# Optimization experiments

Hardware: AMD Instinct MI355X
Metric: run time of the kernel (lower is better)

The kernel has to match this reference:

```python
import jax, jax.numpy as jnp
import numpy as np

EPS = 1e-8
LN_EPS = 1e-5
CAPACITY_BETA = 1.5
IDEAL_CLASSES = 5.0

B, F, E, H, C, G = 8192, 1024, 30, 256, 100, 4096


def setup_inputs() -> dict:
    key = jax.random.key(0)
    ks = jax.random.split(key, 8)
    x = jax.random.normal(ks[0], (B, F), dtype=jnp.float32)
    prototypes = jax.random.normal(ks[1], (E, F), dtype=jnp.float32)
    g_new = jax.random.normal(ks[2], (G,), dtype=jnp.float32)
    g_mem = jax.random.normal(ks[3], (E, G), dtype=jnp.float32)
    class_counts = jax.random.randint(ks[4], (E,), 0, 12, dtype=jnp.int32)
    W1 = jax.random.normal(ks[5], (E, F, H), dtype=jnp.float32) * (1.0 / np.sqrt(F))
    b1 = jnp.zeros((E, H), dtype=jnp.float32)
    gamma = jnp.ones((E, H), dtype=jnp.float32)
    beta = jnp.zeros((E, H), dtype=jnp.float32)
    W2 = jax.random.normal(ks[6], (E, H, C), dtype=jnp.float32) * (1.0 / np.sqrt(H))
    b2 = jnp.zeros((E, C), dtype=jnp.float32)
    return {"x": x, "prototypes": prototypes, "g_new": g_new, "g_mem": g_mem,
            "class_counts": class_counts, "W1": W1, "b1": b1, "gamma": gamma,
            "beta": beta, "W2": W2, "b2": b2}


def _route_scores(x, prototypes, g_new, g_mem, class_counts):
    # Cosine similarity of each sample to each expert prototype: [B, E]
    xn = x / (jnp.linalg.norm(x, axis=-1, keepdims=True) + EPS)
    pn = prototypes / (jnp.linalg.norm(prototypes, axis=-1, keepdims=True) + EPS)
    sim = xn @ pn.T
    # Gradient alignment score per expert (cosine of new grad vs EMA memory), mapped to [0, 1]
    gn = g_new / (jnp.linalg.norm(g_new) + EPS)
    gm = g_mem / (jnp.linalg.norm(g_mem, axis=-1, keepdims=True) + EPS)
    align = 0.5 * (1.0 + gm @ gn)  # [E]
    # Capacity penalty: exponential decay once an expert exceeds its ideal class load
    overload = jnp.maximum(class_counts.astype(jnp.float32) / IDEAL_CLASSES - 1.0, 0.0)
    capacity = jnp.exp(-CAPACITY_BETA * overload)  # [E]
    return sim * (align * capacity)[None, :]  # [B, E]


def reference(x, prototypes, g_new, g_mem, class_counts, W1, b1, gamma, beta, W2, b2):
    scores = _route_scores(x, prototypes, g_new, g_mem, class_counts)  # [B, E]
    assign = jnp.argmax(scores, axis=-1)  # [B] expert id per sample
    # Expert MLP: Linear -> LayerNorm -> GELU -> Linear, evaluated for all experts
    h = jnp.einsum('bf,efh->ebh', x, W1) + b1[:, None, :]  # [E, B, H]
    mu = h.mean(axis=-1, keepdims=True)
    var = ((h - mu) ** 2).mean(axis=-1, keepdims=True)
    ln = (h - mu) * jax.lax.rsqrt(var + LN_EPS) * gamma[:, None, :] + beta[:, None, :]
    a = jax.nn.gelu(ln, approximate=False)  # torch nn.GELU default is exact erf
    logits_all = jnp.einsum('ebh,ehc->ebc', a, W2) + b2[:, None, :]  # [E, B, C]
    # Dispatch: each sample keeps only its assigned expert's logits
    logits = logits_all[assign, jnp.arange(x.shape[0])]  # [B, C]
    return logits
```

## Files before the change

### kernel.cpp

```cpp
#include <hip/hip_runtime.h>
#include <hip/hip_bf16.h>
#include <math.h>
#include <float.h>

namespace {
constexpr int Bn = 8192;
constexpr int Fn = 1024;
constexpr int En = 30;
constexpr int Hn = 256;
constexpr int Cn = 100;
constexpr int Gn = 4096;
constexpr int TILECAP64 = 158;
constexpr int TILECAP32 = 285;
constexpr float EPSF  = 1e-8f;
constexpr float LNEPS = 1e-5f;

typedef _Float16 f16x8 __attribute__((ext_vector_type(8)));
typedef float    f32x4 __attribute__((ext_vector_type(4)));

__device__ __forceinline__ int bswz(int k) { return (k & 7) ^ ((k >> 3) << 2); }
}

#define GLDS16(g, s) __builtin_amdgcn_global_load_lds(                         \
    (const __attribute__((address_space(1))) void*)(uintptr_t)(g),             \
    (__attribute__((address_space(3))) void*)(uintptr_t)(s), 16, 0, 0)

__global__ __launch_bounds__(256) void k_route_w(
    const float* __restrict__ protos,
    const float* __restrict__ g_new,
    const float* __restrict__ g_mem,
    const int* __restrict__ ccounts,
    float* __restrict__ w,
    int* __restrict__ cnt) {
  const int e = blockIdx.x, t = threadIdx.x;
  if (e == 0 && t < 32) cnt[t] = 0;
  float d = 0.f, gm2 = 0.f, gn2 = 0.f, p2 = 0.f;
  for (int g = t; g < Gn; g += 256) {
    float a = g_new[g];
    float m = g_mem[(size_t)e * Gn + g];
    d += a * m; gm2 += m * m; gn2 += a * a;
  }
  for (int f = t; f < Fn; f += 256) {
    float v = protos[(size_t)e * Fn + f];
    p2 += v * v;
  }
#pragma unroll
  for (int m = 1; m < 64; m <<= 1) {
    d   += __shfl_xor(d, m);
    gm2 += __shfl_xor(gm2, m);
    gn2 += __shfl_xor(gn2, m);
    p2  += __shfl_xor(p2, m);
  }
  __shared__ float red[4][4];
  const int lane = t & 63, wid = t >> 6;
  if (lane == 0) { red[wid][0] = d; red[wid][1] = gm2; red[wid][2] = gn2; red[wid][3] = p2; }
  __syncthreads();
  if (t == 0) {
    d   = red[0][0] + red[1][0] + red[2][0] + red[3][0];
    gm2 = red[0][1] + red[1][1] + red[2][1] + red[3][1];
    gn2 = red[0][2] + red[1][2] + red[2][2] + red[3][2];
    p2  = red[0][3] + red[1][3] + red[2][3] + red[3][3];
    float align = 0.5f * (1.0f + d / ((sqrtf(gm2) + EPSF) * (sqrtf(gn2) + EPSF)));
    float over  = fmaxf((float)ccounts[e] / 5.0f - 1.0f, 0.0f);
    float cap   = expf(-1.5f * over);
    w[e] = align * cap / (sqrtf(p2) + EPSF);
  }
}

__global__ __launch_bounds__(256) void k_scores_mfma(
    const float* __restrict__ x,
    const float* __restrict__ protos,
    const float* __restrict__ w,
    int* __restrict__ assign) {
  const int b0 = blockIdx.x * 32;
  extern __shared__ char smem[];
  __shared__ float av_[32][2];
  __shared__ int   ai_[32][2];
  const int t = threadIdx.x, l = t & 63, wv = t >> 6;
  const int mt = wv >> 1, nt = wv & 1;

  const char* asrc[2];
#pragma unroll
  for (int i = 0; i < 2; i++) {
    const int D = i * 256 + t, row = D >> 4, pos = D & 15;
    asrc[i] = (const char*)x + (size_t)(b0 + row) * 4096 + (pos ^ (row & 7)) * 16;
  }
  const char* bsrc[2];
#pragma unroll
  for (int i = 0; i < 2; i++) {
    const int D = i * 256 + t, row = D >> 4, pos = D & 15;
    bsrc[i] = (const char*)protos + (size_t)min(row, En - 1) * 4096 +
              (pos ^ (row & 7)) * 16;
  }

  const int r15 = l & 15, kq = l >> 4;
  int addrA[2][2];
#pragma unroll
  for (int ks = 0; ks < 2; ks++)
#pragma unroll
    for (int i = 0; i < 2; i++) {
      const int row = mt * 16 + r15;
      addrA[ks][i] = row * 256 + (((ks * 8 + kq * 2 + i) ^ (row & 7)) * 16);
    }
  int addrB[2][2];
#pragma unroll
  for (int ks = 0; ks < 2; ks++)
#pragma unroll
    for (int i = 0; i < 2; i++) {
      const int er = nt * 16 + r15;
      addrB[ks][i] = 8192 + er * 256 + (((ks * 8 + kq * 2 + i) ^ (er & 7)) * 16);
    }

  const int  e_w   = nt * 16 + r15;
  const bool valid = (e_w < En);
  const float wsc  = w[min(e_w, En - 1)];

  f32x4 acc = (f32x4){0.f, 0.f, 0.f, 0.f};

  auto stage = [&](int buf, int kt) {
    char* bb = smem + buf * 16384;
#pragma unroll
    for (int i = 0; i < 2; i++)
      GLDS16(asrc[i] + kt * 256, bb + i * 4096 + wv * 1024);
#pragma unroll
    for (int i = 0; i < 2; i++)
      GLDS16(bsrc[i] + kt * 256, bb + 8192 + i * 4096 + wv * 1024);
  };

  stage(0, 0);
  __syncthreads();
  int cur = 0;
  for (int kt = 0; kt < 16; ++kt) {
    if (kt < 15) stage(cur ^ 1, kt + 1);
    const char* bb = smem + cur * 16384;
#pragma unroll
    for (int ks = 0; ks < 2; ks++) {
      f16x8 ah, al;
      {
        float4 a0 = *(const float4*)(bb + addrA[ks][0]);
        float4 a1 = *(const float4*)(bb + addrA[ks][1]);
        float av[8] = {a0.x, a0.y, a0.z, a0.w, a1.x, a1.y, a1.z, a1.w};
#pragma unroll
        for (int j = 0; j < 8; j++) {
          _Float16 hh = (_Float16)av[j];
          ah[j] = hh;
          al[j] = (_Float16)(av[j] - (float)hh);
        }
      }
      f16x8 bh, bl;
      {
        float4 b0v = *(const float4*)(bb + addrB[ks][0]);
        float4 b1v = *(const float4*)(bb + addrB[ks][1]);
        float bv[8] = {b0v.x, b0v.y, b0v.z, b0v.w, b1v.x, b1v.y, b1v.z, b1v.w};
#pragma unroll
        for (int j = 0; j < 8; j++) {
          _Float16 hh = (_Float16)bv[j];
          bh[j] = hh;
          bl[j] = (_Float16)(bv[j] - (float)hh);
        }
      }
      acc = __builtin_amdgcn_mfma_f32_16x16x32_f16(ah, bh, acc, 0, 0, 0);
      acc = __builtin_amdgcn_mfma_f32_16x16x32_f16(al, bh, acc, 0, 0, 0);
      acc = __builtin_amdgcn_mfma_f32_16x16x32_f16(ah, bl, acc, 0, 0, 0);
      acc = __builtin_amdgcn_mfma_f32_16x16x32_f16(al, bl, acc, 0, 0, 0);
    }
    __syncthreads();
    cur ^= 1;
  }

#pragma unroll
  for (int j = 0; j < 4; j++) {
    float best = valid ? acc[j] * wsc : -FLT_MAX;
    int bi = e_w;
#pragma unroll
    for (int m = 1; m < 16; m <<= 1) {
      float ov = __shfl_xor(best, m);
      int   oi = __shfl_xor(bi, m);
      if (ov > best || (ov == best && oi < bi)) { best = ov; bi = oi; }
    }
    if (r15 == 0) {
      const int s = mt * 16 + kq * 4 + j;
      av_[s][nt] = best;
      ai_[s][nt] = bi;
    }
  }
  __syncthreads();
  if (t < 32) {
    const float v0 = av_[t][0], v1 = av_[t][1];
    assign[b0 + t] = (v1 > v0) ? ai_[t][1] : ai_[t][0];
  }
}

__global__ void k_bucket(const int* __restrict__ assign,
                         int* __restrict__ cnt,
                         int* __restrict__ list) {
  const int b = blockIdx.x * 256 + threadIdx.x;
  const int e = assign[b];
  const int pos = atomicAdd(&cnt[e], 1);
  list[e * Bn + pos] = b;
}

__global__ __launch_bounds__(256) void k_planz(
    const int* __restrict__ cnt,
    int* __restrict__ tiles64,
    int* __restrict__ tiles32,
    float* __restrict__ hbuf) {
  const size_t i = ((size_t)blockIdx.x * 256 + threadIdx.x) * 4;
  *(float4*)(hbuf + i) = make_float4(0.f, 0.f, 0.f, 0.f);
  if (blockIdx.x == 0 && threadIdx.x == 0) {
    int tot = 0;
    for (int e = 0; e < En; e++) {
      int nt = (cnt[e] + 63) >> 6;
      for (int k = 0; k < nt && tot + k < TILECAP64; k++)
        tiles64[tot + k] = (e << 16) | k;
      tot += nt;
    }
    for (int k = tot; k < TILECAP64; k++) tiles64[k] = -1;
    tot = 0;
    for (int e = 0; e < En; e++) {
      int nt = (cnt[e] + 31) >> 5;
      for (int k = 0; k < nt && tot + k < TILECAP32; k++)
        tiles32[tot + k] = (e << 16) | k;
      tot += nt;
    }
    for (int k = tot; k < TILECAP32; k++) tiles32[k] = -1;
  }
}

__global__ __launch_bounds__(256) void k_l1_f16(
    const float* __restrict__ x,
    const float* __restrict__ W1,
    const float* __restrict__ b1,
    const int* __restrict__ cnt,
    const int* __restrict__ list,
    const int* __restrict__ tiles,
    float* __restrict__ hbuf) {
  const int tv = tiles[blockIdx.x];
  if (tv < 0) return;
  const int e = tv >> 16, ti = tv & 0xffff;
  const int n = cnt[e];
  const int s0 = ti * 64;
  const int ns = min(64, n - s0);
  const int h0 = blockIdx.y * 128;
  const int k0 = blockIdx.z * 8;

  extern __shared__ char smem[];
  __shared__ int idx[64];
  const int t = threadIdx.x, l = t & 63, w = t >> 6;
  if (t < 64) idx[t] = list[e * Bn + s0 + min(t, ns - 1)];
  __syncthreads();

  const char* asrc[2];
#pragma unroll
  for (int i = 0; i < 2; i++) {
    const int D = i * 256 + t, row = D >> 3, pos = D & 7;
    asrc[i] = (const char*)x + (size_t)idx[row] * 4096 + (pos ^ (row & 7)) * 16;
  }
  const char* bsrc[4];
#pragma unroll
  for (int i = 0; i < 4; i++) {
    const int k  = i * 8 + w * 2 + (l >> 5);
    const int c  = (l & 31) ^ bswz(k);
    bsrc[i] = (const char*)W1 +
              ((size_t)(e * Fn + k) * Hn + h0) * 4 + c * 16;
  }

  const int r15 = l & 15, kq = l >> 4;
  int addrA[4][2];
#pragma unroll
  for (int m = 0; m < 4; m++)
#pragma unroll
    for (int i = 0; i < 2; i++) {
      const int row = m * 16 + r15;
      addrA[m][i] = row * 128 + (((kq * 2 + i) ^ (row & 7)) * 16);
    }
  int addrB[2][8];
#pragma unroll
  for (int nn = 0; nn < 2; nn++)
#pragma unroll
    for (int j = 0; j < 8; j++) {
      const int h = w * 32 + nn * 16 + r15;
      const int kl = kq * 8 + j;
      addrB[nn][j] = 8192 + kl * 512 + (((h >> 2) ^ bswz(kl)) * 16) + (h & 3) * 4;
    }

  f32x4 acc[4][2];
#pragma unroll
  for (int m = 0; m < 4; m++)
#pragma unroll
    for (int nn = 0; nn < 2; nn++) acc[m][nn] = (f32x4){0.f, 0.f, 0.f, 0.f};

  auto stage = [&](int buf, int kt) {
    char* bb = smem + buf * 24576;
#pragma unroll
    for (int i = 0; i < 2; i++)
      GLDS16(asrc[i] + kt * 128, bb + i * 4096 + w * 1024);
#pragma unroll
    for (int i = 0; i < 4; i++)
      GLDS16(bsrc[i] + (size_t)kt * 32768, bb + 8192 + i * 4096 + w * 1024);
  };

  stage(0, k0);
  __syncthreads();
  int cur = 0;
  for (int kt = k0; kt < k0 + 8; ++kt) {
    if (kt < k0 + 7) stage(cur ^ 1, kt + 1);
    const char* bb = smem + cur * 24576;

    f16x8 ah[4], al[4];
#pragma unroll
    for (int m = 0; m < 4; m++) {
      float4 a0 = *(const float4*)(bb + addrA[m][0]);
      float4 a1 = *(const float4*)(bb + addrA[m][1]);
      float av[8] = {a0.x, a0.y, a0.z, a0.w, a1.x, a1.y, a1.z, a1.w};
#pragma unroll
      for (int j = 0; j < 8; j++) {
        _Float16 hh = (_Float16)av[j];
        ah[m][j] = hh;
        al[m][j] = (_Float16)(av[j] - (float)hh);
      }
    }
#pragma unroll
    for (int nn = 0; nn < 2; nn++) {
      float bv[8];
#pragma unroll
      for (int j = 0; j < 8; j++)
        bv[j] = *(const float*)(bb + addrB[nn][j]);
      f16x8 bh, bl;
#pragma unroll
      for (int j = 0; j < 8; j++) {
        _Float16 hh = (_Float16)bv[j];
        bh[j] = hh;
        bl[j] = (_Float16)(bv[j] - (float)hh);
      }
#pragma unroll
      for (int m = 0; m < 4; m++) {
        acc[m][nn] = __builtin_amdgcn_mfma_f32_16x16x32_f16(ah[m], bh, acc[m][nn], 0, 0, 0);
        acc[m][nn] = __builtin_amdgcn_mfma_f32_16x16x32_f16(al[m], bh, acc[m][nn], 0, 0, 0);
        acc[m][nn] = __builtin_amdgcn_mfma_f32_16x16x32_f16(ah[m], bl, acc[m][nn], 0, 0, 0);
      }
    }
    __syncthreads();
    cur ^= 1;
  }

  float bias[2];
#pragma unroll
  for (int nn = 0; nn < 2; nn++)
    bias[nn] = (blockIdx.z == 0)
             ? b1[(size_t)e * Hn + h0 + w * 32 + nn * 16 + r15] : 0.f;
#pragma unroll
  for (int m = 0; m < 4; m++) {
#pragma unroll
    for (int j = 0; j < 4; j++) {
      const int r = m * 16 + kq * 4 + j;
      if (r < ns) {
        float* dst = hbuf + (size_t)idx[r] * Hn + h0 + w * 32;
#pragma unroll
        for (int nn = 0; nn < 2; nn++)
          atomicAdd(dst + nn * 16 + r15, acc[m][nn][j] + bias[nn]);
      }
    }
  }
}

__global__ __launch_bounds__(256) void k_ln2_mfma(
    const float* __restrict__ hbuf,
    const float* __restrict__ gamma,
    const float* __restrict__ beta,
    const float* __restrict__ W2,
    const float* __restrict__ b2,
    const int* __restrict__ cnt,
    const int* __restrict__ list,
    const int* __restrict__ tiles32,
    float* __restrict__ out) {
  const int tv = tiles32[blockIdx.x];
  if (tv < 0) return;
  const int e = tv >> 16, ti = tv & 0xffff;
  const int n = cnt[e];
  const int s0 = ti * 32;
  const int ns = min(32, n - s0);

  __shared__ __align__(16) char aT[32 * 1024];
  __shared__ __align__(16) char bW[2][13312];
  __shared__ int idx[32];

  const int t = threadIdx.x, l = t & 63, w = t >> 6;
  if (t < 32) idx[t] = list[e * Bn + s0 + min(t, ns - 1)];

  const char* w2e = (const char*)W2 + (size_t)e * (Hn * Cn * 4);
  auto stageB = [&](int buf, int kt) {
    const int base = kt * 12800;
    for (int i = w; i < 13; i += 4) {
      int off = base + i * 1024 + l * 16;
      if (off > 102400 - 16) off = 102400 - 16;
      GLDS16(w2e + off, bW[buf] + i * 1024);
    }
  };

  stageB(0, 0);
  __syncthreads();

  const int s = t >> 3, seg = t & 7;
  const int b = idx[s];
  float hv[32];
  float sum = 0.f, sq = 0.f;
  {
    const float* src = hbuf + (size_t)b * Hn + seg * 32;
#pragma unroll
    for (int i = 0; i < 32; i += 4) {
      float4 v = *(const float4*)(src + i);
      hv[i] = v.x; hv[i+1] = v.y; hv[i+2] = v.z; hv[i+3] = v.w;
      sum += v.x + v.y + v.z + v.w;
      sq  += v.x*v.x + v.y*v.y + v.z*v.z + v.w*v.w;
    }
  }
#pragma unroll
  for (int m = 1; m < 8; m <<= 1) { sum += __shfl_xor(sum, m); sq += __shfl_xor(sq, m); }
  const float mu = sum * (1.f / 256.f);
  float var = fmaxf(sq * (1.f / 256.f) - mu * mu, 0.f);
  const float rstd = rsqrtf(var + LNEPS);
#pragma unroll
  for (int i4 = 0; i4 < 8; i4++) {
    float av[4];
#pragma unroll
    for (int j = 0; j < 4; j++) {
      const int hh = seg * 32 + i4 * 4 + j;
      const float g  = gamma[(size_t)e * Hn + hh];
      const float be = beta[(size_t)e * Hn + hh];
      const float ln = (hv[i4 * 4 + j] - mu) * rstd * g + be;
      av[j] = 0.5f * ln * (1.0f + erff(ln * 0.70710678118654752f));
    }
    const int chunk = (seg * 8 + i4) ^ (s & 7);
    *(float4*)(aT + s * 1024 + chunk * 16) = make_float4(av[0], av[1], av[2], av[3]);
  }

  const int r15 = l & 15, kq = l >> 4;
  int addrB[2][8];
#pragma unroll
  for (int ni = 0; ni < 2; ni++) {
    const int nt = w + ni * 4;
    const int c = nt * 16 + r15;
#pragma unroll
    for (int j = 0; j < 8; j++)
      addrB[ni][j] = ((kq * 8 + j) * Cn + c) * 4;
  }

  f32x4 acc[2][2];
#pragma unroll
  for (int m = 0; m < 2; m++)
#pragma unroll
    for (int ni = 0; ni < 2; ni++) acc[m][ni] = (f32x4){0.f, 0.f, 0.f, 0.f};

  __syncthreads();

  int cur = 0;
  for (int kt = 0; kt < 8; ++kt) {
    if (kt < 7) stageB(cur ^ 1, kt + 1);

    f16x8 ah[2], al[2];
#pragma unroll
    for (int m = 0; m < 2; m++) {
      const int row = m * 16 + r15;
      const int c0 = (kt * 8 + kq * 2) ^ (row & 7);
      const int c1 = (kt * 8 + kq * 2 + 1) ^ (row & 7);
      float4 a0 = *(const float4*)(aT + row * 1024 + c0 * 16);
      float4 a1 = *(const float4*)(aT + row * 1024 + c1 * 16);
      float av[8] = {a0.x, a0.y, a0.z, a0.w, a1.x, a1.y, a1.z, a1.w};
#pragma unroll
      for (int j = 0; j < 8; j++) {
        _Float16 hh = (_Float16)av[j];
        ah[m][j] = hh;
        al[m][j] = (_Float16)(av[j] - (float)hh);
      }
    }
#pragma unroll
    for (int ni = 0; ni < 2; ni++) {
      const int nt = w + ni * 4;
      if (nt < 7) {
        float bv[8];
#pragma unroll
        for (int j = 0; j < 8; j++)
          bv[j] = *(const float*)(bW[cur] + addrB[ni][j]);
        f16x8 bh, bl;
#pragma unroll
        for (int j = 0; j < 8; j++) {
          _Float16 hh = (_Float16)bv[j];
          bh[j] = hh;
          bl[j] = (_Float16)(bv[j] - (float)hh);
        }
#pragma unroll
        for (int m = 0; m < 2; m++) {
          acc[m][ni] = __builtin_amdgcn_mfma_f32_16x16x32_f16(ah[m], bh, acc[m][ni], 0, 0, 0);
          acc[m][ni] = __builtin_amdgcn_mfma_f32_16x16x32_f16(al[m], bh, acc[m][ni], 0, 0, 0);
          acc[m][ni] = __builtin_amdgcn_mfma_f32_16x16x32_f16(ah[m], bl, acc[m][ni], 0, 0, 0);
        }
      }
    }
    __syncthreads();
    cur ^= 1;
  }

#pragma unroll
  for (int ni = 0; ni < 2; ni++) {
    const int nt = w + ni * 4;
    if (nt >= 7) continue;
    const int c = nt * 16 + r15;
    if (c >= Cn) continue;
    const float bias = b2[(size_t)e * Cn + c];
#pragma unroll
    for (int m = 0; m < 2; m++) {
#pragma unroll
      for (int j = 0; j < 4; j++) {
        const int r = m * 16 + kq * 4 + j;
        if (r < ns)
          out[(size_t)idx[r] * Cn + c] = acc[m][ni][j] + bias;
      }
    }
  }
}

extern "C" void kernel_launch(void* const* d_in, const int* in_sizes, int n_in,
                              void* d_out, int out_size, void* d_ws, size_t ws_size,
                              hipStream_t stream) {
  const void* x       = d_in[0];
  const void* protos  = d_in[1];
  const void* g_new   = d_in[2];
  const void* g_mem   = d_in[3];
  const int*  ccounts = (const int*)d_in[4];
  const void* W1      = d_in[5];
  const void* b1      = d_in[6];
  const void* gamma   = d_in[7];
  const void* beta    = d_in[8];
  const void* W2      = d_in[9];
  const void* b2      = d_in[10];
  (void)gamma; (void)beta;

  char* ws = (char*)d_ws;
  float* w       = (float*)(ws);
  int*   assign  = (int*)(ws + 512);
  int*   tiles64 = (int*)(ws + 512);
  int*   tiles32 = (int*)(ws + 512 + 1024);
  int*   cnt     = (int*)(ws + 512 + Bn * 4);
  int*   list    = (int*)(ws + 512 + Bn * 4 + 256);
  float* hbuf    = (float*)(ws + 1016576);

  k_route_w<<<dim3(En), 256, 0, stream>>>(
      (const float*)protos, (const float*)g_new, (const float*)g_mem,
      ccounts, w, cnt);
  k_scores_mfma<<<dim3(Bn / 32), 256, 32768, stream>>>(
      (const float*)x, (const float*)protos, w, assign);
  k_bucket<<<Bn / 256, 256, 0, stream>>>(assign, cnt, list);
  k_planz<<<dim3((Bn * Hn) / (256 * 4)), 256, 0, stream>>>(
      cnt, tiles64, tiles32, hbuf);
  k_l1_f16<<<dim3(TILECAP64, 2, 4), 256, 49152, stream>>>(
      (const float*)x, (const float*)W1, (const float*)b1,
      cnt, list, tiles64, hbuf);
  k_ln2_mfma<<<dim3(TILECAP32), 256, 0, stream>>>(
      hbuf, (const float*)gamma, (const float*)beta, (const float*)W2,
      (const float*)b2, cnt, list, tiles32, (float*)d_out);
}
```

Before: 242.8 us.

## Shrink score and layer-2 tiles to 16 rows, halve L1 split-K, aggregate bucket atomics

Result: faster. 222.0 us (-8.6%).

```diff
diff --git a/kernel.cpp b/kernel.cpp
--- a/kernel.cpp
+++ b/kernel.cpp
@@ -11,7 +11,7 @@
 constexpr int Cn = 100;
 constexpr int Gn = 4096;
 constexpr int TILECAP64 = 158;
-constexpr int TILECAP32 = 285;
+constexpr int TILECAP16 = 540;
 constexpr float EPSF  = 1e-8f;
 constexpr float LNEPS = 1e-5f;
 
@@ -72,18 +72,17 @@
     const float* __restrict__ protos,
     const float* __restrict__ w,
     int* __restrict__ assign) {
-  const int b0 = blockIdx.x * 32;
+  const int b0 = blockIdx.x * 16;
   extern __shared__ char smem[];
-  __shared__ float av_[32][2];
-  __shared__ int   ai_[32][2];
+  __shared__ float av_[16][2];
+  __shared__ int   ai_[16][2];
   const int t = threadIdx.x, l = t & 63, wv = t >> 6;
-  const int mt = wv >> 1, nt = wv & 1;
-
-  const char* asrc[2];
-#pragma unroll
-  for (int i = 0; i < 2; i++) {
-    const int D = i * 256 + t, row = D >> 4, pos = D & 15;
-    asrc[i] = (const char*)x + (size_t)(b0 + row) * 4096 + (pos ^ (row & 7)) * 16;
+  const int nt = wv & 1;
+
+  const char* asrc;
+  {
+    const int row = t >> 4, pos = t & 15;
+    asrc = (const char*)x + (size_t)(b0 + row) * 4096 + (pos ^ (row & 7)) * 16;
   }
   const char* bsrc[2];
 #pragma unroll
@@ -98,17 +97,15 @@
 #pragma unroll
   for (int ks = 0; ks < 2; ks++)
 #pragma unroll
-    for (int i = 0; i < 2; i++) {
-      const int row = mt * 16 + r15;
-      addrA[ks][i] = row * 256 + (((ks * 8 + kq * 2 + i) ^ (row & 7)) * 16);
-    }
+    for (int i = 0; i < 2; i++)
+      addrA[ks][i] = r15 * 256 + (((ks * 8 + kq * 2 + i) ^ (r15 & 7)) * 16);
   int addrB[2][2];
 #pragma unroll
   for (int ks = 0; ks < 2; ks++)
 #pragma unroll
     for (int i = 0; i < 2; i++) {
       const int er = nt * 16 + r15;
-      addrB[ks][i] = 8192 + er * 256 + (((ks * 8 + kq * 2 + i) ^ (er & 7)) * 16);
+      addrB[ks][i] = 4096 + er * 256 + (((ks * 8 + kq * 2 + i) ^ (er & 7)) * 16);
     }
 
   const int  e_w   = nt * 16 + r15;
@@ -118,13 +115,11 @@
   f32x4 acc = (f32x4){0.f, 0.f, 0.f, 0.f};
 
   auto stage = [&](int buf, int kt) {
-    char* bb = smem + buf * 16384;
+    char* bb = smem + buf * 12288;
+    GLDS16(asrc + kt * 256, bb + wv * 1024);
 #pragma unroll
     for (int i = 0; i < 2; i++)
-      GLDS16(asrc[i] + kt * 256, bb + i * 4096 + wv * 1024);
-#pragma unroll
-    for (int i = 0; i < 2; i++)
-      GLDS16(bsrc[i] + kt * 256, bb + 8192 + i * 4096 + wv * 1024);
+      GLDS16(bsrc[i] + kt * 256, bb + 4096 + i * 4096 + wv * 1024);
   };
 
   stage(0, 0);
@@ -132,78 +127,90 @@
   int cur = 0;
   for (int kt = 0; kt < 16; ++kt) {
     if (kt < 15) stage(cur ^ 1, kt + 1);
-    const char* bb = smem + cur * 16384;
-#pragma unroll
-    for (int ks = 0; ks < 2; ks++) {
-      f16x8 ah, al;
-      {
-        float4 a0 = *(const float4*)(bb + addrA[ks][0]);
-        float4 a1 = *(const float4*)(bb + addrA[ks][1]);
-        float av[8] = {a0.x, a0.y, a0.z, a0.w, a1.x, a1.y, a1.z, a1.w};
-#pragma unroll
-        for (int j = 0; j < 8; j++) {
-          _Float16 hh = (_Float16)av[j];
-          ah[j] = hh;
-          al[j] = (_Float16)(av[j] - (float)hh);
+    const char* bb = smem + cur * 12288;
+    if (wv < 2) {
+#pragma unroll
+      for (int ks = 0; ks < 2; ks++) {
+        f16x8 ah, al;
+        {
+          float4 a0 = *(const float4*)(bb + addrA[ks][0]);
+          float4 a1 = *(const float4*)(bb + addrA[ks][1]);
+          float av[8] = {a0.x, a0.y, a0.z, a0.w, a1.x, a1.y, a1.z, a1.w};
+#pragma unroll
+          for (int j = 0; j < 8; j++) {
+            _Float16 hh = (_Float16)av[j];
+            ah[j] = hh;
+            al[j] = (_Float16)(av[j] - (float)hh);
+          }
         }
-      }
-      f16x8 bh, bl;
-      {
-        float4 b0v = *(const float4*)(bb + addrB[ks][0]);
-        float4 b1v = *(const float4*)(bb + addrB[ks][1]);
-        float bv[8] = {b0v.x, b0v.y, b0v.z, b0v.w, b1v.x, b1v.y, b1v.z, b1v.w};
-#pragma unroll
-        for (int j = 0; j < 8; j++) {
-          _Float16 hh = (_Float16)bv[j];
-          bh[j] = hh;
-          bl[j] = (_Float16)(bv[j] - (float)hh);
+        f16x8 bh, bl;
+        {
+          float4 b0v = *(const float4*)(bb + addrB[ks][0]);
+          float4 b1v = *(const float4*)(bb + addrB[ks][1]);
+          float bv[8] = {b0v.x, b0v.y, b0v.z, b0v.w, b1v.x, b1v.y, b1v.z, b1v.w};
+#pragma unroll
+          for (int j = 0; j < 8; j++) {
+            _Float16 hh = (_Float16)bv[j];
+            bh[j] = hh;
+            bl[j] = (_Float16)(bv[j] - (float)hh);
+          }
         }
-      }
-      acc = __builtin_amdgcn_mfma_f32_16x16x32_f16(ah, bh, acc, 0, 0, 0);
-      acc = __builtin_amdgcn_mfma_f32_16x16x32_f16(al, bh, acc, 0, 0, 0);
-      acc = __builtin_amdgcn_mfma_f32_16x16x32_f16(ah, bl, acc, 0, 0, 0);
-      acc = __builtin_amdgcn_mfma_f32_16x16x32_f16(al, bl, acc, 0, 0, 0);
+        acc = __builtin_amdgcn_mfma_f32_16x16x32_f16(ah, bh, acc, 0, 0, 0);
+        acc = __builtin_amdgcn_mfma_f32_16x16x32_f16(al, bh, acc, 0, 0, 0);
+        acc = __builtin_amdgcn_mfma_f32_16x16x32_f16(ah, bl, acc, 0, 0, 0);
+        acc = __builtin_amdgcn_mfma_f32_16x16x32_f16(al, bl, acc, 0, 0, 0);
+      }
     }
     __syncthreads();
     cur ^= 1;
   }
 
-#pragma unroll
-  for (int j = 0; j < 4; j++) {
-    float best = valid ? acc[j] * wsc : -FLT_MAX;
-    int bi = e_w;
-#pragma unroll
-    for (int m = 1; m < 16; m <<= 1) {
-      float ov = __shfl_xor(best, m);
-      int   oi = __shfl_xor(bi, m);
-      if (ov > best || (ov == best && oi < bi)) { best = ov; bi = oi; }
-    }
-    if (r15 == 0) {
-      const int s = mt * 16 + kq * 4 + j;
-      av_[s][nt] = best;
-      ai_[s][nt] = bi;
-    }
-  }
-  __syncthreads();
-  if (t < 32) {
+  if (wv < 2) {
+#pragma unroll
+    for (int j = 0; j < 4; j++) {
+      float best = valid ? acc[j] * wsc : -FLT_MAX;
+      int bi = e_w;
+#pragma unroll
+      for (int m = 1; m < 16; m <<= 1) {
+        float ov = __shfl_xor(best, m);
+        int   oi = __shfl_xor(bi, m);
+        if (ov > best || (ov == best && oi < bi)) { best = ov; bi = oi; }
+      }
+      if (r15 == 0) {
+        const int s = kq * 4 + j;
+        av_[s][nt] = best;
+        ai_[s][nt] = bi;
+      }
+    }
+  }
+  __syncthreads();
+  if (t < 16) {
     const float v0 = av_[t][0], v1 = av_[t][1];
     assign[b0 + t] = (v1 > v0) ? ai_[t][1] : ai_[t][0];
   }
 }
 
-__global__ void k_bucket(const int* __restrict__ assign,
-                         int* __restrict__ cnt,
-                         int* __restrict__ list) {
-  const int b = blockIdx.x * 256 + threadIdx.x;
+__global__ __launch_bounds__(256) void k_bucket(
+    const int* __restrict__ assign,
+    int* __restrict__ cnt,
+    int* __restrict__ list) {
+  __shared__ int lcnt[32], lbase[32];
+  const int t = threadIdx.x;
+  const int b = blockIdx.x * 256 + t;
+  if (t < 32) lcnt[t] = 0;
+  __syncthreads();
   const int e = assign[b];
-  const int pos = atomicAdd(&cnt[e], 1);
-  list[e * Bn + pos] = b;
+  const int lpos = atomicAdd(&lcnt[e], 1);
+  __syncthreads();
+  if (t < 32) lbase[t] = (lcnt[t] > 0) ? atomicAdd(&cnt[t], lcnt[t]) : 0;
+  __syncthreads();
+  list[e * Bn + lbase[e] + lpos] = b;
 }
 
 __global__ __launch_bounds__(256) void k_planz(
     const int* __restrict__ cnt,
     int* __restrict__ tiles64,
-    int* __restrict__ tiles32,
+    int* __restrict__ tiles16,
     float* __restrict__ hbuf) {
   const size_t i = ((size_t)blockIdx.x * 256 + threadIdx.x) * 4;
   *(float4*)(hbuf + i) = make_float4(0.f, 0.f, 0.f, 0.f);
@@ -218,12 +225,12 @@
     for (int k = tot; k < TILECAP64; k++) tiles64[k] = -1;
     tot = 0;
     for (int e = 0; e < En; e++) {
-      int nt = (cnt[e] + 31) >> 5;
-      for (int k = 0; k < nt && tot + k < TILECAP32; k++)
-        tiles32[tot + k] = (e << 16) | k;
+      int nt = (cnt[e] + 15) >> 4;
+      for (int k = 0; k < nt && tot + k < TILECAP16; k++)
+        tiles16[tot + k] = (e << 16) | k;
       tot += nt;
     }
-    for (int k = tot; k < TILECAP32; k++) tiles32[k] = -1;
+    for (int k = tot; k < TILECAP16; k++) tiles16[k] = -1;
   }
 }
 
@@ -242,7 +249,7 @@
   const int s0 = ti * 64;
   const int ns = min(64, n - s0);
   const int h0 = blockIdx.y * 128;
-  const int k0 = blockIdx.z * 8;
+  const int k0 = blockIdx.z * 16;
 
   extern __shared__ char smem[];
   __shared__ int idx[64];
@@ -303,8 +310,8 @@
   stage(0, k0);
   __syncthreads();
   int cur = 0;
-  for (int kt = k0; kt < k0 + 8; ++kt) {
-    if (kt < k0 + 7) stage(cur ^ 1, kt + 1);
+  for (int kt = k0; kt < k0 + 16; ++kt) {
+    if (kt < k0 + 15) stage(cur ^ 1, kt + 1);
     const char* bb = smem + cur * 24576;
 
     f16x8 ah[4], al[4];
@@ -372,21 +379,21 @@
     const float* __restrict__ b2,
     const int* __restrict__ cnt,
     const int* __restrict__ list,
-    const int* __restrict__ tiles32,
+    const int* __restrict__ tiles16,
     float* __restrict__ out) {
-  const int tv = tiles32[blockIdx.x];
+  const int tv = tiles16[blockIdx.x];
   if (tv < 0) return;
   const int e = tv >> 16, ti = tv & 0xffff;
   const int n = cnt[e];
-  const int s0 = ti * 32;
-  const int ns = min(32, n - s0);
-
-  __shared__ __align__(16) char aT[32 * 1024];
+  const int s0 = ti * 16;
+  const int ns = min(16, n - s0);
+
+  __shared__ __align__(16) char aT[16 * 1024];
   __shared__ __align__(16) char bW[2][13312];
-  __shared__ int idx[32];
+  __shared__ int idx[16];
 
   const int t = threadIdx.x, l = t & 63, w = t >> 6;
-  if (t < 32) idx[t] = list[e * Bn + s0 + min(t, ns - 1)];
+  if (t < 16) idx[t] = list[e * Bn + s0 + min(t, ns - 1)];
 
   const char* w2e = (const char*)W2 + (size_t)e * (Hn * Cn * 4);
   auto stageB = [&](int buf, int kt) {
@@ -401,14 +408,14 @@
   stageB(0, 0);
   __syncthreads();
 
-  const int s = t >> 3, seg = t & 7;
+  const int s = t >> 4, seg = t & 15;
   const int b = idx[s];
-  float hv[32];
+  float hv[16];
   float sum = 0.f, sq = 0.f;
   {
-    const float* src = hbuf + (size_t)b * Hn + seg * 32;
-#pragma unroll
-    for (int i = 0; i < 32; i += 4) {
+    const float* src = hbuf + (size_t)b * Hn + seg * 16;
+#pragma unroll
+    for (int i = 0; i < 16; i += 4) {
       float4 v = *(const float4*)(src + i);
       hv[i] = v.x; hv[i+1] = v.y; hv[i+2] = v.z; hv[i+3] = v.w;
       sum += v.x + v.y + v.z + v.w;
@@ -416,22 +423,22 @@
     }
   }
 #pragma unroll
-  for (int m = 1; m < 8; m <<= 1) { sum += __shfl_xor(sum, m); sq += __shfl_xor(sq, m); }
+  for (int m = 1; m < 16; m <<= 1) { sum += __shfl_xor(sum, m); sq += __shfl_xor(sq, m); }
   const float mu = sum * (1.f / 256.f);
   float var = fmaxf(sq * (1.f / 256.f) - mu * mu, 0.f);
   const float rstd = rsqrtf(var + LNEPS);
 #pragma unroll
-  for (int i4 = 0; i4 < 8; i4++) {
+  for (int i4 = 0; i4 < 4; i4++) {
     float av[4];
 #pragma unroll
     for (int j = 0; j < 4; j++) {
-      const int hh = seg * 32 + i4 * 4 + j;
+      const int hh = seg * 16 + i4 * 4 + j;
       const float g  = gamma[(size_t)e * Hn + hh];
       const float be = beta[(size_t)e * Hn + hh];
       const float ln = (hv[i4 * 4 + j] - mu) * rstd * g + be;
       av[j] = 0.5f * ln * (1.0f + erff(ln * 0.70710678118654752f));
     }
-    const int chunk = (seg * 8 + i4) ^ (s & 7);
+    const int chunk = (seg * 4 + i4) ^ (s & 7);
     *(float4*)(aT + s * 1024 + chunk * 16) = make_float4(av[0], av[1], av[2], av[3]);
   }
 
@@ -446,11 +453,9 @@
       addrB[ni][j] = ((kq * 8 + j) * Cn + c) * 4;
   }
 
-  f32x4 acc[2][2];
-#pragma unroll
-  for (int m = 0; m < 2; m++)
-#pragma unroll
-    for (int ni = 0; ni < 2; ni++) acc[m][ni] = (f32x4){0.f, 0.f, 0.f, 0.f};
+  f32x4 acc[2];
+  acc[0] = (f32x4){0.f, 0.f, 0.f, 0.f};
+  acc[1] = (f32x4){0.f, 0.f, 0.f, 0.f};
 
   __syncthreads();
 
@@ -458,20 +463,18 @@
   for (int kt = 0; kt < 8; ++kt) {
     if (kt < 7) stageB(cur ^ 1, kt + 1);
 
-    f16x8 ah[2], al[2];
-#pragma unroll
-    for (int m = 0; m < 2; m++) {
-      const int row = m * 16 + r15;
-      const int c0 = (kt * 8 + kq * 2) ^ (row & 7);
-      const int c1 = (kt * 8 + kq * 2 + 1) ^ (row & 7);
-      float4 a0 = *(const float4*)(aT + row * 1024 + c0 * 16);
-      float4 a1 = *(const float4*)(aT + row * 1024 + c1 * 16);
+    f16x8 ah, al;
+    {
+      const int c0 = (kt * 8 + kq * 2) ^ (r15 & 7);
+      const int c1 = (kt * 8 + kq * 2 + 1) ^ (r15 & 7);
+      float4 a0 = *(const float4*)(aT + r15 * 1024 + c0 * 16);
+      float4 a1 = *(const float4*)(aT + r15 * 1024 + c1 * 16);
       float av[8] = {a0.x, a0.y, a0.z, a0.w, a1.x, a1.y, a1.z, a1.w};
 #pragma unroll
       for (int j = 0; j < 8; j++) {
         _Float16 hh = (_Float16)av[j];
-        ah[m][j] = hh;
-        al[m][j] = (_Float16)(av[j] - (float)hh);
+        ah[j] = hh;
+        al[j] = (_Float16)(av[j] - (float)hh);
       }
     }
 #pragma unroll
@@ -489,12 +492,9 @@
           bh[j] = hh;
           bl[j] = (_Float16)(bv[j] - (float)hh);
         }
-#pragma unroll
-        for (int m = 0; m < 2; m++) {
-          acc[m][ni] = __builtin_amdgcn_mfma_f32_16x16x32_f16(ah[m], bh, acc[m][ni], 0, 0, 0);
-          acc[m][ni] = __builtin_amdgcn_mfma_f32_16x16x32_f16(al[m], bh, acc[m][ni], 0, 0, 0);
-          acc[m][ni] = __builtin_amdgcn_mfma_f32_16x16x32_f16(ah[m], bl, acc[m][ni], 0, 0, 0);
-        }
+        acc[ni] = __builtin_amdgcn_mfma_f32_16x16x32_f16(ah, bh, acc[ni], 0, 0, 0);
+        acc[ni] = __builtin_amdgcn_mfma_f32_16x16x32_f16(al, bh, acc[ni], 0, 0, 0);
+        acc[ni] = __builtin_amdgcn_mfma_f32_16x16x32_f16(ah, bl, acc[ni], 0, 0, 0);
       }
     }
     __syncthreads();
@@ -509,13 +509,10 @@
     if (c >= Cn) continue;
     const float bias = b2[(size_t)e * Cn + c];
 #pragma unroll
-    for (int m = 0; m < 2; m++) {
-#pragma unroll
-      for (int j = 0; j < 4; j++) {
-        const int r = m * 16 + kq * 4 + j;
-        if (r < ns)
-          out[(size_t)idx[r] * Cn + c] = acc[m][ni][j] + bias;
-      }
+    for (int j = 0; j < 4; j++) {
+      const int r = kq * 4 + j;
+      if (r < ns)
+        out[(size_t)idx[r] * Cn + c] = acc[ni][j] + bias;
     }
   }
 }
@@ -534,13 +531,12 @@
   const void* beta    = d_in[8];
   const void* W2      = d_in[9];
   const void* b2      = d_in[10];
-  (void)gamma; (void)beta;
 
   char* ws = (char*)d_ws;
   float* w       = (float*)(ws);
   int*   assign  = (int*)(ws + 512);
   int*   tiles64 = (int*)(ws + 512);
-  int*   tiles32 = (int*)(ws + 512 + 1024);
+  int*   tiles16 = (int*)(ws + 512 + 1024);
   int*   cnt     = (int*)(ws + 512 + Bn * 4);
   int*   list    = (int*)(ws + 512 + Bn * 4 + 256);
   float* hbuf    = (float*)(ws + 1016576);
@@ -548,15 +544,15 @@
   k_route_w<<<dim3(En), 256, 0, stream>>>(
       (const float*)protos, (const float*)g_new, (const float*)g_mem,
       ccounts, w, cnt);
-  k_scores_mfma<<<dim3(Bn / 32), 256, 32768, stream>>>(
+  k_scores_mfma<<<dim3(Bn / 16), 256, 24576, stream>>>(
       (const float*)x, (const float*)protos, w, assign);
   k_bucket<<<Bn / 256, 256, 0, stream>>>(assign, cnt, list);
   k_planz<<<dim3((Bn * Hn) / (256 * 4)), 256, 0, stream>>>(
-      cnt, tiles64, tiles32, hbuf);
-  k_l1_f16<<<dim3(TILECAP64, 2, 4), 256, 49152, stream>>>(
+      cnt, tiles64, tiles16, hbuf);
+  k_l1_f16<<<dim3(TILECAP64, 2, 2), 256, 49152, stream>>>(
       (const float*)x, (const float*)W1, (const float*)b1,
       cnt, list, tiles64, hbuf);
-  k_ln2_mfma<<<dim3(TILECAP32), 256, 0, stream>>>(
+  k_ln2_mfma<<<dim3(TILECAP16), 256, 0, stream>>>(
       hbuf, (const float*)gamma, (const float*)beta, (const float*)W2,
-      (const float*)b2, cnt, list, tiles32, (float*)d_out);
-}
+      (const float*)b2, cnt, list, tiles16, (float*)d_out);
+}
```
